# Performance work log

Hardware: AMD Instinct MI355X
Metric: run time of the kernel (lower is better)

Reference implementation:

```python
import jax, jax.numpy as jnp
import numpy as np


def conv1x1(x, W, b):
    # 1x1 conv == channel mixing: [O,C] x [B,C,H,W] -> [B,O,H,W]
    return jnp.einsum('oc,bchw->bohw', W, x) + b[None, :, None, None]


def _fmm(x, x_th, Wk_rgb, bk_rgb, Wk_th, bk_th, Wv_rgb, bv_rgb, Wv_th, bv_th,
         gamma_rgb, gamma_th, gamma2_rgb, gamma2_th):
    b, c, w, h = x.shape
    n = w * h
    x_k    = conv1x1(x,    Wk_rgb, bk_rgb).reshape(b, c, n)
    x_th_k = conv1x1(x_th, Wk_th,  bk_th ).reshape(b, c, n)
    x_v    = conv1x1(x,    Wv_rgb, bv_rgb).reshape(b, c, n)
    x_v_th = conv1x1(x_th, Wv_th,  bv_th ).reshape(b, c, n)

    # spatial attention: sim[b, n, m] = x_th_k^T @ x_k, softmax over m
    sim = jax.nn.softmax(jnp.einsum('bcn,bcm->bnm', x_th_k, x_k), axis=-1)
    x_1    = jnp.einsum('bcn,bnm->bcm', x_v,    sim).reshape(b, c, w, h)
    x_th_1 = jnp.einsum('bcn,bnm->bcm', x_v_th, sim).reshape(b, c, w, h)
    x_1    = x_1 * gamma_rgb + x
    x_th_1 = x_th_1 * gamma_th + x_th

    # channel attention with max-subtraction (note: uses value projections, not x_1)
    energy = jnp.einsum('bcn,bdn->bcd', x_v_th, x_v)  # [b, c, c]
    sim_c = jax.nn.softmax(jnp.max(energy, axis=-1, keepdims=True) - energy, axis=-1)
    x_2    = jnp.einsum('bcd,bdn->bcn', sim_c, x_v   ).reshape(b, c, w, h)
    x_th_2 = jnp.einsum('bcd,bdn->bcn', sim_c, x_v_th).reshape(b, c, w, h)
    x_2    = gamma2_rgb * x_2    + x_1
    x_th_2 = gamma2_th  * x_th_2 + x_th_1
    return x_2, x_th_2


def setup_inputs() -> dict:
    key = jax.random.key(0)
    ks = jax.random.split(key, 12)
    b, c, w, h = 4, 256, 64, 64
    scale = 1.0 / np.sqrt(c)
    f32 = jnp.float32
    d = {
        'x':    jax.random.normal(ks[0], (b, c, w, h), f32),
        'x_th': jax.random.normal(ks[1], (b, c, w, h), f32),
        'Wk_rgb': jax.random.normal(ks[2], (c, c), f32) * scale,
        'bk_rgb': jax.random.normal(ks[3], (c,), f32) * 0.01,
        'Wk_th':  jax.random.normal(ks[4], (c, c), f32) * scale,
        'bk_th':  jax.random.normal(ks[5], (c,), f32) * 0.01,
        'Wv_rgb': jax.random.normal(ks[6], (c, c), f32) * scale,
        'bv_rgb': jax.random.normal(ks[7], (c,), f32) * 0.01,
        'Wv_th':  jax.random.normal(ks[8], (c, c), f32) * scale,
        'bv_th':  jax.random.normal(ks[9], (c,), f32) * 0.01,
        # gammas init to 0 in the original; use small nonzero so both branches are exercised
        'gamma_rgb':  jnp.full((1,), 0.5, f32),
        'gamma_th':   jnp.full((1,), 0.4, f32),
        'gamma2_rgb': jnp.full((1,), 0.3, f32),
        'gamma2_th':  jnp.full((1,), 0.2, f32),
    }
    return d


def reference(x, x_th, Wk_rgb, bk_rgb, Wk_th, bk_th, Wv_rgb, bv_rgb, Wv_th, bv_th,
              gamma_rgb, gamma_th, gamma2_rgb, gamma2_th):
    return _fmm(x, x_th, Wk_rgb, bk_rgb, Wk_th, bk_th, Wv_rgb, bv_rgb, Wv_th, bv_th,
                gamma_rgb, gamma_th, gamma2_rgb, gamma2_th)
```

## Files before the change

### kernel.cpp

```cpp
#include <hip/hip_runtime.h>

typedef unsigned short u16;
typedef __attribute__((ext_vector_type(8))) _Float16 f16x8;
typedef __attribute__((ext_vector_type(4))) float f32x4;

#define DEVINL __device__ __forceinline__

DEVINL u16 f2h_u(float f) { _Float16 h = (_Float16)f; return __builtin_bit_cast(unsigned short, h); }
DEVINL float h2f_u(u16 h) { return (float)__builtin_bit_cast(_Float16, h); }

DEVINL f16x8 ldfrag(const u16* p) {
    int4 d = *(const int4*)p;
    return __builtin_bit_cast(f16x8, d);
}

DEVINL void glds16(const u16* g, u16* l) {
    __builtin_amdgcn_global_load_lds(
        (const __attribute__((address_space(1))) unsigned int*)g,
        (__attribute__((address_space(3))) unsigned int*)l, 16, 0, 0);
}

#define CFENCE asm volatile("" ::: "memory")
#define VMCNT8 asm volatile("s_waitcnt vmcnt(8)" ::: "memory")
#define VMCNT0 asm volatile("s_waitcnt vmcnt(0)" ::: "memory")
#define LGKM0  asm volatile("s_waitcnt lgkmcnt(0)" ::: "memory")

static const long CN  = 256L * 4096L;
static const long PtE = 4096L * 4096L;

DEVINL void gemm_core(const u16* __restrict__ Ag, int lda,
                      const u16* __restrict__ Bg, int ldb,
                      int kOff, int kLen, u16* As, u16* Bs, f32x4 (&acc)[4][4])
{
    int tid = threadIdx.x;
    int lane = tid & 63, w = tid >> 6;
    int wr = w >> 1, wc = w & 1;
    int kg = lane >> 4, rl = lane & 15;
    int l8 = lane >> 3, c8 = lane & 7;

    int srow = w * 32 + l8;
    int scol = (c8 ^ l8) * 8;
    const u16* aS = Ag + (size_t)srow * lda + kOff + scol;
    const u16* bS = Bg + (size_t)srow * ldb + kOff + scol;
    int dOff = w * 2048;

    int rl7 = rl & 7;
    int e0 = (kg ^ rl7) * 8;
    int e1 = e0 ^ 32;
    int aRow = (wr * 64 + rl) * 64;
    int bRow = (wc * 64 + rl) * 64;

    int nt = kLen >> 6;
#pragma unroll
    for (int q = 0; q < 4; ++q) {
        glds16(aS + (size_t)q * 8 * lda, As + dOff + q * 512);
        glds16(bS + (size_t)q * 8 * ldb, Bs + dOff + q * 512);
    }
#pragma unroll
    for (int q = 0; q < 4; ++q) {
        glds16(aS + (size_t)q * 8 * lda + 64, As + 8192 + dOff + q * 512);
        glds16(bS + (size_t)q * 8 * ldb + 64, Bs + 8192 + dOff + q * 512);
    }

    for (int t = 0; t < nt; ++t) {
        const u16* Ab = As + (t & 1) * 8192;
        const u16* Bb = Bs + (t & 1) * 8192;
        if (t + 1 < nt) { VMCNT8; } else { VMCNT0; }
        __builtin_amdgcn_s_barrier();
        CFENCE;
        f16x8 a0[4], b0[4], a1[4], b1[4];
#pragma unroll
        for (int i = 0; i < 4; ++i) a0[i] = ldfrag(&Ab[aRow + i * 1024 + e0]);
#pragma unroll
        for (int i = 0; i < 4; ++i) b0[i] = ldfrag(&Bb[bRow + i * 1024 + e0]);
#pragma unroll
        for (int i = 0; i < 4; ++i) a1[i] = ldfrag(&Ab[aRow + i * 1024 + e1]);
#pragma unroll
        for (int i = 0; i < 4; ++i) b1[i] = ldfrag(&Bb[bRow + i * 1024 + e1]);
        __builtin_amdgcn_s_setprio(1);
#pragma unroll
        for (int i = 0; i < 4; ++i)
#pragma unroll
            for (int j = 0; j < 4; ++j)
                acc[i][j] = __builtin_amdgcn_mfma_f32_16x16x32_f16(a0[i], b0[j], acc[i][j], 0, 0, 0);
#pragma unroll
        for (int i = 0; i < 4; ++i)
#pragma unroll
            for (int j = 0; j < 4; ++j)
                acc[i][j] = __builtin_amdgcn_mfma_f32_16x16x32_f16(a1[i], b1[j], acc[i][j], 0, 0, 0);
        __builtin_amdgcn_s_setprio(0);
        LGKM0;
        __builtin_amdgcn_s_barrier();
        CFENCE;
        if (t + 2 < nt) {
            const u16* aN = aS + (size_t)(t + 2) * 64;
            const u16* bN = bS + (size_t)(t + 2) * 64;
            u16* Ad = As + (t & 1) * 8192 + dOff;
            u16* Bd = Bs + (t & 1) * 8192 + dOff;
#pragma unroll
            for (int q = 0; q < 4; ++q) {
                glds16(aN + (size_t)q * 8 * lda, Ad + q * 512);
                glds16(bN + (size_t)q * 8 * ldb, Bd + q * 512);
            }
        }
    }
}

DEVINL void mergeMS(float& m, float& s, float om, float os) {
    float nm = fmaxf(m, om);
    s = s * __expf(m - nm) + os * __expf(om - nm);
    m = nm;
}

__launch_bounds__(256, 2)
__global__ void st_gemm(const u16* __restrict__ Kt, const u16* __restrict__ Ktth,
                        u16* __restrict__ StH,
                        float* __restrict__ pmax, float* __restrict__ psum)
{
    __shared__ __align__(16) u16 As[2 * 8192];
    __shared__ __align__(16) u16 Bs[2 * 8192];
    int P = blockIdx.x;
    int L = (P & 7) * 512 + (P >> 3);
    int b = L >> 10, yb = (L >> 5) & 31, xb = L & 31;
    const u16* A = Kt   + (long)b * CN + (size_t)yb * 128 * 256;
    const u16* B = Ktth + (long)b * CN + (size_t)xb * 128 * 256;
    u16* out = StH + (long)b * PtE;
    int rowBase = yb * 128, colBase = xb * 128;

    f32x4 acc[4][4];
#pragma unroll
    for (int i = 0; i < 4; ++i)
#pragma unroll
        for (int j = 0; j < 4; ++j) acc[i][j] = (f32x4){0.f, 0.f, 0.f, 0.f};

    gemm_core(A, 256, B, 256, 0, 256, As, Bs, acc);

    int lane = threadIdx.x & 63, w = threadIdx.x >> 6;
    int wr = w >> 1, wc = w & 1, kg = lane >> 4, rl = lane & 15;

    float tm[4], ts[4];
#pragma unroll
    for (int j = 0; j < 4; ++j) { tm[j] = -3.0e38f; ts[j] = 0.f; }

#pragma unroll
    for (int i = 0; i < 4; ++i) {
        int row0 = rowBase + wr * 64 + i * 16 + kg * 4;
#pragma unroll
        for (int j = 0; j < 4; ++j) {
            int col = colBase + wc * 64 + j * 16 + rl;
            f32x4 v = acc[i][j];
#pragma unroll
            for (int r = 0; r < 4; ++r) {
                u16 h = f2h_u(v[r]);
                out[(size_t)(row0 + r) * 4096 + col] = h;
                float x = h2f_u(h);
                float nm = fmaxf(tm[j], x);
                ts[j] = ts[j] * __expf(tm[j] - nm) + __expf(x - nm);
                tm[j] = nm;
            }
        }
    }
#pragma unroll
    for (int j = 0; j < 4; ++j) {
        mergeMS(tm[j], ts[j], __shfl_xor(tm[j], 16, 64), __shfl_xor(ts[j], 16, 64));
        mergeMS(tm[j], ts[j], __shfl_xor(tm[j], 32, 64), __shfl_xor(ts[j], 32, 64));
    }
    float* red = (float*)As;
    __syncthreads();
    if (wr == 1 && lane < 16) {
#pragma unroll
        for (int j = 0; j < 4; ++j) {
            red[((wc * 4 + j) * 16 + rl) * 2 + 0] = tm[j];
            red[((wc * 4 + j) * 16 + rl) * 2 + 1] = ts[j];
        }
    }
    __syncthreads();
    if (wr == 0 && lane < 16) {
#pragma unroll
        for (int j = 0; j < 4; ++j) {
            mergeMS(tm[j], ts[j], red[((wc * 4 + j) * 16 + rl) * 2 + 0],
                                  red[((wc * 4 + j) * 16 + rl) * 2 + 1]);
            int col = colBase + wc * 64 + j * 16 + rl;
            long idx = ((long)b * 32 + yb) * 4096 + col;
            pmax[idx] = tm[j];
            psum[idx] = ts[j];
        }
    }
}

__global__ void stats_combine(const float* __restrict__ pmax, const float* __restrict__ psum,
                              float* __restrict__ cmax, float* __restrict__ crcp)
{
    int b = blockIdx.y;
    int col = blockIdx.x * 256 + threadIdx.x;
    const float* pm = pmax + (long)b * 32 * 4096 + col;
    const float* ps = psum + (long)b * 32 * 4096 + col;
    float m = -3.0e38f, s = 0.f;
    for (int i = 0; i < 32; ++i) mergeMS(m, s, pm[i * 4096], ps[i * 4096]);
    cmax[b * 4096 + col] = m;
    crcp[b * 4096 + col] = 1.f / s;
}

template<int EPI>
__launch_bounds__(256, 2)
__global__ void gemm512(const u16* __restrict__ A, int lda, long sAz,
                        const u16* __restrict__ B, int ldb, long sBz,
                        int K, int splitK, int zshift,
                        void* outv, int ldo, long sOz)
{
    __shared__ __align__(16) u16 As[2 * 8192];
    __shared__ __align__(16) u16 Bs[2 * 8192];
    int z = blockIdx.z;
    int bq = z >> zshift, s = z & ((1 << zshift) - 1);
    int kOff = s * splitK, kLen = splitK;
    A += sAz * bq; B += sBz * bq;
    long zo = sOz * bq;
    int rowBase = blockIdx.y * 128, colBase = blockIdx.x * 128;
    f32x4 acc[4][4];
#pragma unroll
    for (int i = 0; i < 4; ++i)
#pragma unroll
        for (int j = 0; j < 4; ++j) acc[i][j] = (f32x4){0.f, 0.f, 0.f, 0.f};

    gemm_core(A + (size_t)rowBase * lda, lda, B + (size_t)colBase * ldb, ldb, kOff, kLen, As, Bs, acc);

    int lane = threadIdx.x & 63, w = threadIdx.x >> 6;
    int wr = w >> 1, wc = w & 1, kg = lane >> 4, rl = lane & 15;
    float* outf = (float*)outv;
#pragma unroll
    for (int i = 0; i < 4; ++i) {
        int row0 = rowBase + wr * 64 + i * 16 + kg * 4;
#pragma unroll
        for (int j = 0; j < 4; ++j) {
            int col = colBase + wc * 64 + j * 16 + rl;
            f32x4 v = acc[i][j];
#pragma unroll
            for (int r = 0; r < 4; ++r) {
                size_t o = (size_t)(row0 + r) * ldo + col;
                atomicAdd(&outf[zo + o], v[r]);
            }
        }
    }
}

__launch_bounds__(256, 2)
__global__ void proj_all(const u16* __restrict__ xT, const u16* __restrict__ xthT,
                         const u16* __restrict__ wts,
                         const float* __restrict__ b0, const float* __restrict__ b1,
                         const float* __restrict__ b2, const float* __restrict__ b3,
                         u16* o0, u16* o1, u16* o2, u16* o3)
{
    __shared__ __align__(16) u16 As[2 * 8192];
    __shared__ __align__(16) u16 Bs[2 * 8192];
    int z = blockIdx.z, b = z >> 2, t = z & 3;
    const u16* A = ((t & 1) ? xthT : xT) + (long)b * CN;
    const u16* B = wts + t * 65536;
    u16* out = t == 0 ? o0 + (long)b * CN : t == 1 ? o1 + (long)b * CN
             : t == 2 ? o2 + (long)b * 2 * CN : o3 + (long)b * 2 * CN;
    int rowBase = blockIdx.y * 128, colBase = blockIdx.x * 128;
    f32x4 acc[4][4];
#pragma unroll
    for (int i = 0; i < 4; ++i)
#pragma unroll
        for (int j = 0; j < 4; ++j) acc[i][j] = (f32x4){0.f, 0.f, 0.f, 0.f};

    gemm_core(A + (size_t)rowBase * 256, 256, B + (size_t)colBase * 256, 256, 0, 256, As, Bs, acc);

    const float* bias = t == 0 ? b0 : t == 1 ? b1 : t == 2 ? b2 : b3;
    int lane = threadIdx.x & 63, w = threadIdx.x >> 6;
    int wr = w >> 1, wc = w & 1, kg = lane >> 4, rl = lane & 15;
#pragma unroll
    for (int i = 0; i < 4; ++i) {
        int row0 = rowBase + wr * 64 + i * 16 + kg * 4;
#pragma unroll
        for (int j = 0; j < 4; ++j) {
            int col = colBase + wc * 64 + j * 16 + rl;
            f32x4 v = acc[i][j];
#pragma unroll
            for (int r = 0; r < 4; ++r)
                out[(size_t)(row0 + r) * 256 + col] = f2h_u(v[r] + bias[col]);
        }
    }
}

template<int MODE>
__launch_bounds__(256, 2)
__global__ void gemm_fused(const u16* __restrict__ Abase, const u16* __restrict__ Bbase,
                           const float* __restrict__ g0p, const float* __restrict__ g1p,
                           const float* __restrict__ src0, const float* __restrict__ src1,
                           float* __restrict__ out0, float* __restrict__ out1)
{
    __shared__ __align__(16) u16 As[2 * 8192];
    __shared__ __align__(16) u16 Bs[2 * 8192];
    int P = blockIdx.x;
    int L = (P & 7) * 64 + (P >> 3);
    int b, n, y, t;
    const u16 *A, *B;
    int lda, ldb, K;
    if (MODE == 0) {
        b = L >> 7; n = (L >> 2) & 31; y = (L >> 1) & 1; t = L & 1;
        A = Abase + ((long)b * 2 + t) * CN;  lda = 4096;
        B = Bbase + (long)b * PtE;           ldb = 4096;
        K = 4096;
    } else {
        b = L >> 7; t = (L >> 6) & 1; n = (L >> 1) & 31; y = L & 1;
        A = Abase + (long)b * 65536;         lda = 256;
        B = Bbase + ((long)b * 2 + t) * CN;  ldb = 256;
        K = 256;
    }
    const float* src = (t ? src1 : src0) + (long)b * CN;
    float* out = (t ? out1 : out0) + (long)b * CN;
    int rowBase = y * 128, colBase = n * 128;

    f32x4 acc[4][4];
#pragma unroll
    for (int i = 0; i < 4; ++i)
#pragma unroll
        for (int j = 0; j < 4; ++j) acc[i][j] = (f32x4){0.f, 0.f, 0.f, 0.f};

    gemm_core(A + (size_t)rowBase * lda, lda, B + (size_t)colBase * ldb, ldb, 0, K, As, Bs, acc);

    float gamma = t ? *g1p : *g0p;
    int lane = threadIdx.x & 63, w = threadIdx.x >> 6;
    int wr = w >> 1, wc = w & 1, kg = lane >> 4, rl = lane & 15;
#pragma unroll
    for (int i = 0; i < 4; ++i) {
        int row0 = rowBase + wr * 64 + i * 16 + kg * 4;
#pragma unroll
        for (int j = 0; j < 4; ++j) {
            int col = colBase + wc * 64 + j * 16 + rl;
            f32x4 v = acc[i][j];
#pragma unroll
            for (int r = 0; r < 4; ++r) {
                int row = row0 + r;
                out[(size_t)row * 4096 + col] = gamma * v[r] + src[(size_t)row * 4096 + col];
            }
        }
    }
}

__global__ void tr_f32_h2(const float* __restrict__ in0, const float* __restrict__ in1,
                          u16* __restrict__ out0, u16* __restrict__ out1)
{
    int z = blockIdx.z, b = z & 3;
    const float* in = ((z >> 2) ? in1 : in0) + (long)b * CN;
    u16* out = ((z >> 2) ? out1 : out0) + (long)b * CN;
    __shared__ u16 s[64 * 65];
    int tx = threadIdx.x & 63, tw = threadIdx.x >> 6;
    int r0 = blockIdx.y * 64, c0 = blockIdx.x * 64;
#pragma unroll
    for (int p = 0; p < 16; ++p) {
        int r = tw + p * 4;
        s[tx * 65 + r] = f2h_u(in[(size_t)(r0 + r) * 4096 + c0 + tx]);
    }
    __syncthreads();
#pragma unroll
    for (int p = 0; p < 16; ++p) {
        int rr = tw + p * 4;
        out[(size_t)(c0 + rr) * 256 + r0 + tx] = s[rr * 65 + tx];
    }
}

__global__ void tr_h_h(const u16* __restrict__ in, u16* __restrict__ out,
                       int R, int NC_, long sIn, long sOut)
{
    in += (long)blockIdx.z * sIn; out += (long)blockIdx.z * sOut;
    __shared__ u16 s[64 * 65];
    int tx = threadIdx.x & 63, tw = threadIdx.x >> 6;
    int r0 = blockIdx.y * 64, c0 = blockIdx.x * 64;
#pragma unroll
    for (int p = 0; p < 16; ++p) {
        int r = tw + p * 4;
        s[tx * 65 + r] = in[(size_t)(r0 + r) * NC_ + c0 + tx];
    }
    __syncthreads();
#pragma unroll
    for (int p = 0; p < 16; ++p) {
        int rr = tw + p * 4;
        out[(size_t)(c0 + rr) * R + r0 + tx] = s[rr * 65 + tx];
    }
}

__global__ void cvt_w_kernel(const float* __restrict__ w0, const float* __restrict__ w1,
                             const float* __restrict__ w2, const float* __restrict__ w3,
                             u16* __restrict__ out)
{
    int i = blockIdx.x * 256 + threadIdx.x;
    const float* w = (i < 65536) ? w0 : (i < 131072) ? w1 : (i < 196608) ? w2 : w3;
    out[i] = f2h_u(w[i & 65535]);
}

__global__ void pt8_kernel(u16* St, const float* __restrict__ cmax,
                           const float* __restrict__ crcp)
{
    int b = blockIdx.z;
    St += (long)b * PtE;
    cmax += b * 4096; crcp += b * 4096;
    int m = blockIdx.y;
    int c0 = (blockIdx.x * 256 + threadIdx.x) * 8;
    size_t o = (size_t)m * 4096 + c0;
    f16x8 hv = __builtin_bit_cast(f16x8, *(const int4*)(St + o));
    union { u16 q[8]; int4 v; } pk;
#pragma unroll
    for (int j = 0; j < 8; ++j)
        pk.q[j] = f2h_u(__expf((float)hv[j] - cmax[c0 + j]) * crcp[c0 + j]);
    *(int4*)(St + o) = pk.v;
}

DEVINL float blockReduce(float v, int op) {
    __shared__ float s[4];
#pragma unroll
    for (int o = 32; o; o >>= 1) {
        float t = __shfl_xor(v, o, 64);
        v = op ? (v + t) : fmaxf(v, t);
    }
    __syncthreads();
    if ((threadIdx.x & 63) == 0) s[threadIdx.x >> 6] = v;
    __syncthreads();
    return op ? (s[0] + s[1] + s[2] + s[3]) : fmaxf(fmaxf(s[0], s[1]), fmaxf(s[2], s[3]));
}

__global__ void simc_kernel(const float* __restrict__ E, u16* __restrict__ simc)
{
    int bb = blockIdx.y;
    const float* Eb = E + bb * 65536;
    u16* sc = simc + bb * 65536;
    int c = blockIdx.x, d = threadIdx.x;
    float e = Eb[c * 256 + d];
    float rmax = blockReduce(e, 0);
    float v = rmax - e;
    float vmax = blockReduce(v, 0);
    float p = __expf(v - vmax);
    float s = blockReduce(p, 1);
    sc[c * 256 + d] = f2h_u(p / s);
}

extern "C" void kernel_launch(void* const* d_in, const int* in_sizes, int n_in,
                              void* d_out, int out_size, void* d_ws, size_t ws_size,
                              hipStream_t stream)
{
    const float* x      = (const float*)d_in[0];
    const float* xth    = (const float*)d_in[1];
    const float* Wk_rgb = (const float*)d_in[2];
    const float* bk_rgb = (const float*)d_in[3];
    const float* Wk_th  = (const float*)d_in[4];
    const float* bk_th  = (const float*)d_in[5];
    const float* Wv_rgb = (const float*)d_in[6];
    const float* bv_rgb = (const float*)d_in[7];
    const float* Wv_th  = (const float*)d_in[8];
    const float* bv_th  = (const float*)d_in[9];
    const float* g1r = (const float*)d_in[10];
    const float* g1t = (const float*)d_in[11];
    const float* g2r = (const float*)d_in[12];
    const float* g2t = (const float*)d_in[13];

    u16* wts   = (u16*)d_ws;
    u16* Kt    = wts + 4 * 65536;
    u16* Ktth  = Kt + 4 * CN;
    u16* Vt2   = Ktth + 4 * CN;
    u16* V2    = Vt2 + 8 * CN;
    u16* StH   = V2 + 8 * CN;
    u16* simc   = Kt;
    float* E    = (float*)(Kt + 4 * 65536);
    u16* xT    = StH;
    u16* xthT  = xT + 4 * CN;

    float* outX2  = (float*)d_out;
    float* outXt2 = outX2 + 4 * CN;

    float* pmax = outX2;
    float* psum = pmax + 4 * 32 * 4096;
    float* cmax = psum + 4 * 32 * 4096;
    float* crcp = cmax + 4 * 4096;

    cvt_w_kernel<<<1024, 256, 0, stream>>>(Wk_rgb, Wk_th, Wv_rgb, Wv_th, wts);
    tr_f32_h2<<<dim3(64, 4, 8), 256, 0, stream>>>(x, xth, xT, xthT);

    proj_all<<<dim3(2, 32, 16), 256, 0, stream>>>(xT, xthT, wts,
        bk_rgb, bk_th, bv_rgb, bv_th, Kt, Ktth, Vt2, Vt2 + CN);

    tr_h_h<<<dim3(4, 64, 8), 256, 0, stream>>>(Vt2, V2, 4096, 256, CN, CN);

    st_gemm<<<4096, 256, 0, stream>>>(Kt, Ktth, StH, pmax, psum);
    stats_combine<<<dim3(16, 4), 256, 0, stream>>>(pmax, psum, cmax, crcp);
    pt8_kernel<<<dim3(2, 4096, 4), 256, 0, stream>>>(StH, cmax, crcp);

    gemm_fused<0><<<512, 256, 0, stream>>>(
        V2, StH, g1r, g1t, x, xth, outX2, outXt2);

    (void)hipMemsetAsync(E, 0, 4 * 65536 * sizeof(float), stream);
    gemm512<2><<<dim3(2, 2, 128), 256, 0, stream>>>(
        V2 + CN, 4096, 2 * CN, V2, 4096, 2 * CN,
        4096, 128, 5, E, 256, 65536);
    simc_kernel<<<dim3(256, 4), 256, 0, stream>>>(E, simc);

    gemm_fused<1><<<512, 256, 0, stream>>>(
        simc, Vt2, g2r, g2t, outX2, outXt2, outX2, outXt2);
}
```

Baseline: 269.9 us.

## Fuse softmax normalization into PV GEMM B-operand staging, drop pt8 pass

Removes the separate pass that read the 4096x4096 fp16 score matrix, exponentiated and normalized it, and wrote it back. The PV GEMM now loads raw scores into registers, applies exp2 with precomputed max*log2e and reciprocal sums, and stores the result to shared memory with its own pipelined load schedule. The column-stat epilogue in st_gemm changes from online exp updates to a max pass followed by a sum pass, and all exponentials use exp2. This saves a full read/write of the large score tensor in exchange for more register pressure and ALU work inside the GEMM loop.

```diff
diff --git a/kernel.cpp b/kernel.cpp
--- a/kernel.cpp
+++ b/kernel.cpp
@@ -1,13 +1,17 @@
 #include <hip/hip_runtime.h>
 
 typedef unsigned short u16;
+typedef unsigned int u32;
 typedef __attribute__((ext_vector_type(8))) _Float16 f16x8;
+typedef __attribute__((ext_vector_type(2))) _Float16 f16x2;
 typedef __attribute__((ext_vector_type(4))) float f32x4;
 
 #define DEVINL __device__ __forceinline__
+#define LOG2E 1.44269504f
 
 DEVINL u16 f2h_u(float f) { _Float16 h = (_Float16)f; return __builtin_bit_cast(unsigned short, h); }
 DEVINL float h2f_u(u16 h) { return (float)__builtin_bit_cast(_Float16, h); }
+DEVINL float ex2(float x) { return __builtin_amdgcn_exp2f(x); }
 
 DEVINL f16x8 ldfrag(const u16* p) {
     int4 d = *(const int4*)p;
@@ -20,10 +24,12 @@
         (__attribute__((address_space(3))) unsigned int*)l, 16, 0, 0);
 }
 
-#define CFENCE asm volatile("" ::: "memory")
-#define VMCNT8 asm volatile("s_waitcnt vmcnt(8)" ::: "memory")
-#define VMCNT0 asm volatile("s_waitcnt vmcnt(0)" ::: "memory")
-#define LGKM0  asm volatile("s_waitcnt lgkmcnt(0)" ::: "memory")
+#define CFENCE  asm volatile("" ::: "memory")
+#define VMCNT12 asm volatile("s_waitcnt vmcnt(12)" ::: "memory")
+#define VMCNT8  asm volatile("s_waitcnt vmcnt(8)" ::: "memory")
+#define VMCNT4  asm volatile("s_waitcnt vmcnt(4)" ::: "memory")
+#define VMCNT0  asm volatile("s_waitcnt vmcnt(0)" ::: "memory")
+#define LGKM0   asm volatile("s_waitcnt lgkmcnt(0)" ::: "memory")
 
 static const long CN  = 256L * 4096L;
 static const long PtE = 4096L * 4096L;
@@ -108,7 +114,7 @@
 
 DEVINL void mergeMS(float& m, float& s, float om, float os) {
     float nm = fmaxf(m, om);
-    s = s * __expf(m - nm) + os * __expf(om - nm);
+    s = s * ex2((m - nm) * LOG2E) + os * ex2((om - nm) * LOG2E);
     m = nm;
 }
 
@@ -138,10 +144,7 @@
     int lane = threadIdx.x & 63, w = threadIdx.x >> 6;
     int wr = w >> 1, wc = w & 1, kg = lane >> 4, rl = lane & 15;
 
-    float tm[4], ts[4];
-#pragma unroll
-    for (int j = 0; j < 4; ++j) { tm[j] = -3.0e38f; ts[j] = 0.f; }
-
+    float vr[4][4][4];
 #pragma unroll
     for (int i = 0; i < 4; ++i) {
         int row0 = rowBase + wr * 64 + i * 16 + kg * 4;
@@ -153,12 +156,24 @@
             for (int r = 0; r < 4; ++r) {
                 u16 h = f2h_u(v[r]);
                 out[(size_t)(row0 + r) * 4096 + col] = h;
-                float x = h2f_u(h);
-                float nm = fmaxf(tm[j], x);
-                ts[j] = ts[j] * __expf(tm[j] - nm) + __expf(x - nm);
-                tm[j] = nm;
+                vr[i][j][r] = h2f_u(h);
             }
         }
+    }
+    float tm[4], ts[4];
+#pragma unroll
+    for (int j = 0; j < 4; ++j) {
+        float m = vr[0][j][0];
+#pragma unroll
+        for (int i = 0; i < 4; ++i)
+#pragma unroll
+            for (int r = 0; r < 4; ++r) m = fmaxf(m, vr[i][j][r]);
+        float mk = m * LOG2E, s = 0.f;
+#pragma unroll
+        for (int i = 0; i < 4; ++i)
+#pragma unroll
+            for (int r = 0; r < 4; ++r) s += ex2(fmaf(vr[i][j][r], LOG2E, -mk));
+        tm[j] = m; ts[j] = s;
     }
 #pragma unroll
     for (int j = 0; j < 4; ++j) {
@@ -189,7 +204,7 @@
 }
 
 __global__ void stats_combine(const float* __restrict__ pmax, const float* __restrict__ psum,
-                              float* __restrict__ cmax, float* __restrict__ crcp)
+                              float* __restrict__ cmK, float* __restrict__ crcp)
 {
     int b = blockIdx.y;
     int col = blockIdx.x * 256 + threadIdx.x;
@@ -197,22 +212,176 @@
     const float* ps = psum + (long)b * 32 * 4096 + col;
     float m = -3.0e38f, s = 0.f;
     for (int i = 0; i < 32; ++i) mergeMS(m, s, pm[i * 4096], ps[i * 4096]);
-    cmax[b * 4096 + col] = m;
+    cmK[b * 4096 + col] = m * LOG2E;
     crcp[b * 4096 + col] = 1.f / s;
 }
 
-template<int EPI>
+DEVINL int4 expquad(int4 rg, const float* cm8, const float* cr8) {
+    f16x8 hv = __builtin_bit_cast(f16x8, rg);
+    u32 o[4];
+#pragma unroll
+    for (int p = 0; p < 4; ++p) {
+        float a0 = fmaf((float)hv[2 * p],     LOG2E, -cm8[2 * p]);
+        float a1 = fmaf((float)hv[2 * p + 1], LOG2E, -cm8[2 * p + 1]);
+        float q0 = ex2(a0) * cr8[2 * p];
+        float q1 = ex2(a1) * cr8[2 * p + 1];
+        o[p] = __builtin_bit_cast(u32, __builtin_amdgcn_cvt_pkrtz(q0, q1));
+    }
+    return make_int4(o[0], o[1], o[2], o[3]);
+}
+
 __launch_bounds__(256, 2)
-__global__ void gemm512(const u16* __restrict__ A, int lda, long sAz,
-                        const u16* __restrict__ B, int ldb, long sBz,
-                        int K, int splitK, int zshift,
-                        void* outv, int ldo, long sOz)
+__global__ void pv_gemm(const u16* __restrict__ V2, const u16* __restrict__ StH,
+                        const float* __restrict__ cmKb, const float* __restrict__ crcpb,
+                        const float* __restrict__ g0p, const float* __restrict__ g1p,
+                        const float* __restrict__ src0, const float* __restrict__ src1,
+                        float* __restrict__ out0, float* __restrict__ out1)
+{
+    __shared__ __align__(16) u16 As[2 * 8192];
+    __shared__ __align__(16) u16 Bs[2 * 8192];
+    int P = blockIdx.x;
+    int L = (P & 7) * 64 + (P >> 3);
+    int b = L >> 7, n = (L >> 2) & 31, y = (L >> 1) & 1, t = L & 1;
+    const u16* A = V2 + ((long)b * 2 + t) * CN + (size_t)(y * 128) * 4096;
+    const u16* B = StH + (long)b * PtE + (size_t)(n * 128) * 4096;
+    const float* cm = cmKb + b * 4096;
+    const float* cr = crcpb + b * 4096;
+
+    int tid = threadIdx.x;
+    int lane = tid & 63, w = tid >> 6;
+    int wr = w >> 1, wc = w & 1;
+    int kg = lane >> 4, rl = lane & 15;
+    int l8 = lane >> 3, c8 = lane & 7;
+
+    int srow = w * 32 + l8;
+    int scol = (c8 ^ l8) * 8;
+    const u16* aS = A + (size_t)srow * 4096 + scol;
+    const u16* bS = B + (size_t)srow * 4096 + scol;
+    int dOff = w * 2048;
+
+    int rl7 = rl & 7;
+    int e0 = (kg ^ rl7) * 8;
+    int e1 = e0 ^ 32;
+    int aRow = (wr * 64 + rl) * 64;
+    int bRow = (wc * 64 + rl) * 64;
+
+    f32x4 acc[4][4];
+#pragma unroll
+    for (int i = 0; i < 4; ++i)
+#pragma unroll
+        for (int j = 0; j < 4; ++j) acc[i][j] = (f32x4){0.f, 0.f, 0.f, 0.f};
+
+    int4 br0, br1, br2, br3;
+    float4 cmv0, cmv1, crv0, crv1;
+
+    auto BG_LOAD = [&](int T) {
+        const u16* bp = bS + (size_t)T * 64;
+        br0 = *(const int4*)(bp);
+        br1 = *(const int4*)(bp + (size_t)8 * 4096);
+        br2 = *(const int4*)(bp + (size_t)16 * 4096);
+        br3 = *(const int4*)(bp + (size_t)24 * 4096);
+        cmv0 = *(const float4*)(cm + T * 64 + scol);
+        cmv1 = *(const float4*)(cm + T * 64 + scol + 4);
+        crv0 = *(const float4*)(cr + T * 64 + scol);
+        crv1 = *(const float4*)(cr + T * 64 + scol + 4);
+    };
+    auto AG = [&](int T) {
+#pragma unroll
+        for (int q = 0; q < 4; ++q)
+            glds16(aS + (size_t)T * 64 + (size_t)q * 8 * 4096,
+                   As + (T & 1) * 8192 + dOff + q * 512);
+    };
+    auto BSTAGE = [&](int T) {
+        float cm8[8] = {cmv0.x, cmv0.y, cmv0.z, cmv0.w, cmv1.x, cmv1.y, cmv1.z, cmv1.w};
+        float cr8[8] = {crv0.x, crv0.y, crv0.z, crv0.w, crv1.x, crv1.y, crv1.z, crv1.w};
+        u16* bd = Bs + (T & 1) * 8192 + dOff + lane * 8;
+        *(int4*)(bd)        = expquad(br0, cm8, cr8);
+        *(int4*)(bd + 512)  = expquad(br1, cm8, cr8);
+        *(int4*)(bd + 1024) = expquad(br2, cm8, cr8);
+        *(int4*)(bd + 1536) = expquad(br3, cm8, cr8);
+    };
+
+    BG_LOAD(0); CFENCE;
+    AG(0);      CFENCE;
+    VMCNT4;
+    BSTAGE(0);  CFENCE;
+    BG_LOAD(1); CFENCE;
+    AG(1);
+    LGKM0;
+
+    const int nt = 64;
+    for (int t2 = 0; t2 < nt; ++t2) {
+        if (t2 + 1 < nt) { VMCNT12; } else { VMCNT0; }
+        __builtin_amdgcn_s_barrier();
+        CFENCE;
+        const u16* Ab = As + (t2 & 1) * 8192;
+        const u16* Bb = Bs + (t2 & 1) * 8192;
+        f16x8 a0[4], b0[4], a1[4], b1[4];
+#pragma unroll
+        for (int i = 0; i < 4; ++i) a0[i] = ldfrag(&Ab[aRow + i * 1024 + e0]);
+#pragma unroll
+        for (int i = 0; i < 4; ++i) b0[i] = ldfrag(&Bb[bRow + i * 1024 + e0]);
+#pragma unroll
+        for (int i = 0; i < 4; ++i) a1[i] = ldfrag(&Ab[aRow + i * 1024 + e1]);
+#pragma unroll
+        for (int i = 0; i < 4; ++i) b1[i] = ldfrag(&Bb[bRow + i * 1024 + e1]);
+        __builtin_amdgcn_s_setprio(1);
+#pragma unroll
+        for (int i = 0; i < 4; ++i)
+#pragma unroll
+            for (int j = 0; j < 4; ++j)
+                acc[i][j] = __builtin_amdgcn_mfma_f32_16x16x32_f16(a0[i], b0[j], acc[i][j], 0, 0, 0);
+#pragma unroll
+        for (int i = 0; i < 4; ++i)
+#pragma unroll
+            for (int j = 0; j < 4; ++j)
+                acc[i][j] = __builtin_amdgcn_mfma_f32_16x16x32_f16(a1[i], b1[j], acc[i][j], 0, 0, 0);
+        __builtin_amdgcn_s_setprio(0);
+        if (t2 + 1 < nt) {
+            VMCNT4;
+            BSTAGE(t2 + 1);
+            CFENCE;
+        }
+        LGKM0;
+        __builtin_amdgcn_s_barrier();
+        CFENCE;
+        if (t2 + 2 < nt) {
+            BG_LOAD(t2 + 2); CFENCE;
+            AG(t2 + 2);
+        }
+    }
+
+    float gamma = t ? *g1p : *g0p;
+    const float* src = (t ? src1 : src0) + (long)b * CN;
+    float* out = (t ? out1 : out0) + (long)b * CN;
+    int rowBase = y * 128, colBase = n * 128;
+#pragma unroll
+    for (int i = 0; i < 4; ++i) {
+        int row0 = rowBase + wr * 64 + i * 16 + kg * 4;
+#pragma unroll
+        for (int j = 0; j < 4; ++j) {
+            int col = colBase + wc * 64 + j * 16 + rl;
+            f32x4 v = acc[i][j];
+#pragma unroll
+            for (int r = 0; r < 4; ++r) {
+                int row = row0 + r;
+                out[(size_t)row * 4096 + col] = gamma * v[r] + src[(size_t)row * 4096 + col];
+            }
+        }
+    }
+}
+
+__launch_bounds__(256, 2)
+__global__ void gemm_splitk(const u16* __restrict__ A, int lda, long sAz,
+                            const u16* __restrict__ B, int ldb, long sBz,
+                            int splitK, int zshift,
+                            float* __restrict__ outf, int ldo, long sOz)
 {
     __shared__ __align__(16) u16 As[2 * 8192];
     __shared__ __align__(16) u16 Bs[2 * 8192];
     int z = blockIdx.z;
     int bq = z >> zshift, s = z & ((1 << zshift) - 1);
-    int kOff = s * splitK, kLen = splitK;
+    int kOff = s * splitK;
     A += sAz * bq; B += sBz * bq;
     long zo = sOz * bq;
     int rowBase = blockIdx.y * 128, colBase = blockIdx.x * 128;
@@ -222,11 +391,10 @@
 #pragma unroll
         for (int j = 0; j < 4; ++j) acc[i][j] = (f32x4){0.f, 0.f, 0.f, 0.f};
 
-    gemm_core(A + (size_t)rowBase * lda, lda, B + (size_t)colBase * ldb, ldb, kOff, kLen, As, Bs, acc);
+    gemm_core(A + (size_t)rowBase * lda, lda, B + (size_t)colBase * ldb, ldb, kOff, splitK, As, Bs, acc);
 
     int lane = threadIdx.x & 63, w = threadIdx.x >> 6;
     int wr = w >> 1, wc = w & 1, kg = lane >> 4, rl = lane & 15;
-    float* outf = (float*)outv;
 #pragma unroll
     for (int i = 0; i < 4; ++i) {
         int row0 = rowBase + wr * 64 + i * 16 + kg * 4;
@@ -235,10 +403,8 @@
             int col = colBase + wc * 64 + j * 16 + rl;
             f32x4 v = acc[i][j];
 #pragma unroll
-            for (int r = 0; r < 4; ++r) {
-                size_t o = (size_t)(row0 + r) * ldo + col;
-                atomicAdd(&outf[zo + o], v[r]);
-            }
+            for (int r = 0; r < 4; ++r)
+                atomicAdd(&outf[zo + (size_t)(row0 + r) * ldo + col], v[r]);
         }
     }
 }
@@ -283,31 +449,19 @@
     }
 }
 
-template<int MODE>
 __launch_bounds__(256, 2)
-__global__ void gemm_fused(const u16* __restrict__ Abase, const u16* __restrict__ Bbase,
-                           const float* __restrict__ g0p, const float* __restrict__ g1p,
-                           const float* __restrict__ src0, const float* __restrict__ src1,
-                           float* __restrict__ out0, float* __restrict__ out1)
+__global__ void ch_gemm(const u16* __restrict__ simcb, const u16* __restrict__ Vt2,
+                        const float* __restrict__ g0p, const float* __restrict__ g1p,
+                        const float* __restrict__ src0, const float* __restrict__ src1,
+                        float* __restrict__ out0, float* __restrict__ out1)
 {
     __shared__ __align__(16) u16 As[2 * 8192];
     __shared__ __align__(16) u16 Bs[2 * 8192];
     int P = blockIdx.x;
     int L = (P & 7) * 64 + (P >> 3);
-    int b, n, y, t;
-    const u16 *A, *B;
-    int lda, ldb, K;
-    if (MODE == 0) {
-        b = L >> 7; n = (L >> 2) & 31; y = (L >> 1) & 1; t = L & 1;
-        A = Abase + ((long)b * 2 + t) * CN;  lda = 4096;
-        B = Bbase + (long)b * PtE;           ldb = 4096;
-        K = 4096;
-    } else {
-        b = L >> 7; t = (L >> 6) & 1; n = (L >> 1) & 31; y = L & 1;
-        A = Abase + (long)b * 65536;         lda = 256;
-        B = Bbase + ((long)b * 2 + t) * CN;  ldb = 256;
-        K = 256;
-    }
+    int b = L >> 7, t = (L >> 6) & 1, n = (L >> 1) & 31, y = L & 1;
+    const u16* A = simcb + (long)b * 65536;
+    const u16* B = Vt2 + ((long)b * 2 + t) * CN;
     const float* src = (t ? src1 : src0) + (long)b * CN;
     float* out = (t ? out1 : out0) + (long)b * CN;
     int rowBase = y * 128, colBase = n * 128;
@@ -318,7 +472,7 @@
 #pragma unroll
         for (int j = 0; j < 4; ++j) acc[i][j] = (f32x4){0.f, 0.f, 0.f, 0.f};
 
-    gemm_core(A + (size_t)rowBase * lda, lda, B + (size_t)colBase * ldb, ldb, 0, K, As, Bs, acc);
+    gemm_core(A + (size_t)rowBase * 256, 256, B + (size_t)colBase * 256, 256, 0, 256, As, Bs, acc);
 
     float gamma = t ? *g1p : *g0p;
     int lane = threadIdx.x & 63, w = threadIdx.x >> 6;
@@ -388,23 +542,6 @@
     int i = blockIdx.x * 256 + threadIdx.x;
     const float* w = (i < 65536) ? w0 : (i < 131072) ? w1 : (i < 196608) ? w2 : w3;
     out[i] = f2h_u(w[i & 65535]);
-}
-
-__global__ void pt8_kernel(u16* St, const float* __restrict__ cmax,
-                           const float* __restrict__ crcp)
-{
-    int b = blockIdx.z;
-    St += (long)b * PtE;
-    cmax += b * 4096; crcp += b * 4096;
-    int m = blockIdx.y;
-    int c0 = (blockIdx.x * 256 + threadIdx.x) * 8;
-    size_t o = (size_t)m * 4096 + c0;
-    f16x8 hv = __builtin_bit_cast(f16x8, *(const int4*)(St + o));
-    union { u16 q[8]; int4 v; } pk;
-#pragma unroll
-    for (int j = 0; j < 8; ++j)
-        pk.q[j] = f2h_u(__expf((float)hv[j] - cmax[c0 + j]) * crcp[c0 + j]);
-    *(int4*)(St + o) = pk.v;
 }
 
 DEVINL float blockReduce(float v, int op) {
@@ -462,6 +599,8 @@
     u16* StH   = V2 + 8 * CN;
     u16* simc   = Kt;
     float* E    = (float*)(Kt + 4 * 65536);
+    float* cmK  = E + 4 * 65536;
+    float* crcp = cmK + 4 * 4096;
     u16* xT    = StH;
     u16* xthT  = xT + 4 * CN;
 
@@ -470,8 +609,6 @@
 
     float* pmax = outX2;
     float* psum = pmax + 4 * 32 * 4096;
-    float* cmax = psum + 4 * 32 * 4096;
-    float* crcp = cmax + 4 * 4096;
 
     cvt_w_kernel<<<1024, 256, 0, stream>>>(Wk_rgb, Wk_th, Wv_rgb, Wv_th, wts);
     tr_f32_h2<<<dim3(64, 4, 8), 256, 0, stream>>>(x, xth, xT, xthT);
@@ -482,18 +619,17 @@
     tr_h_h<<<dim3(4, 64, 8), 256, 0, stream>>>(Vt2, V2, 4096, 256, CN, CN);
 
     st_gemm<<<4096, 256, 0, stream>>>(Kt, Ktth, StH, pmax, psum);
-    stats_combine<<<dim3(16, 4), 256, 0, stream>>>(pmax, psum, cmax, crcp);
-    pt8_kernel<<<dim3(2, 4096, 4), 256, 0, stream>>>(StH, cmax, crcp);
-
-    gemm_fused<0><<<512, 256, 0, stream>>>(
-        V2, StH, g1r, g1t, x, xth, outX2, outXt2);
+    stats_combine<<<dim3(16, 4), 256, 0, stream>>>(pmax, psum, cmK, crcp);
+
+    pv_gemm<<<512, 256, 0, stream>>>(
+        V2, StH, cmK, crcp, g1r, g1t, x, xth, outX2, outXt2);
 
     (void)hipMemsetAsync(E, 0, 4 * 65536 * sizeof(float), stream);
-    gemm512<2><<<dim3(2, 2, 128), 256, 0, stream>>>(
+    gemm_splitk<<<dim3(2, 2, 128), 256, 0, stream>>>(
         V2 + CN, 4096, 2 * CN, V2, 4096, 2 * CN,
-        4096, 128, 5, E, 256, 65536);
+        128, 5, E, 256, 65536);
     simc_kernel<<<dim3(256, 4), 256, 0, stream>>>(E, simc);
 
-    gemm_fused<1><<<512, 256, 0, stream>>>(
+    ch_gemm<<<512, 256, 0, stream>>>(
         simc, Vt2, g2r, g2t, outX2, outXt2, outX2, outXt2);
 }
```

Result: no change. 274.2 us (+1.6%).
